# Kernel optimization log

Measured on AMD Instinct MI355X. Metric: run time of the kernel, lower is better.

The kernel has to match this reference:

```python
import jax, jax.numpy as jnp
import numpy as np
import math

B, N, D, H, L, F, K = 4, 256, 768, 32, 12, 3072, 128
HD = D // H
ATOM_TYPES = 64
EDGE_TYPES = ATOM_TYPES * ATOM_TYPES
BLOCKS = 1
SQRT_2PI = math.sqrt(2.0 * math.pi)


def _ln(x, g, b):
    m = jnp.mean(x, -1, keepdims=True)
    v = jnp.mean((x - m) ** 2, -1, keepdims=True)
    return (x - m) * jax.lax.rsqrt(v + 1e-5) * g + b


def _gelu(x):
    return jax.nn.gelu(x, approximate=False)


def setup_inputs():
    key = jax.random.key(0)
    ks = iter(jax.random.split(key, 64))
    def nrm(shape, s=0.02):
        return jax.random.normal(next(ks), shape, jnp.float32) * s
    inp = dict(
        atoms=jax.random.randint(next(ks), (B, N), 0, ATOM_TYPES),
        tags=jax.random.randint(next(ks), (B, N), 0, 3),
        pos=jax.random.normal(next(ks), (B, N, 3), jnp.float32) * 3.0,
        real_mask=jnp.ones((B, N), dtype=bool),
        atom_emb=nrm((ATOM_TYPES, D)),
        tag_emb=nrm((3, D)),
        gbf_means=jax.random.uniform(next(ks), (K,), jnp.float32, 0.0, 3.0),
        gbf_stds=jax.random.uniform(next(ks), (K,), jnp.float32, 0.0, 3.0),
        gbf_mul=jnp.ones((EDGE_TYPES, 1), jnp.float32),
        gbf_bias=jnp.zeros((EDGE_TYPES, 1), jnp.float32),
        bp_w1=nrm((K, K)), bp_b1=jnp.zeros((K,), jnp.float32),
        bp_w2=nrm((H, K)), bp_b2=jnp.zeros((H,), jnp.float32),
        ep_w=nrm((D, K)), ep_b=jnp.zeros((D,), jnp.float32),
        ln1_g=jnp.ones((L, D), jnp.float32), ln1_b=jnp.zeros((L, D), jnp.float32),
        wqkv=nrm((L, 3 * D, D)), bqkv=jnp.zeros((L, 3 * D), jnp.float32),
        wo=nrm((L, D, D)), bo=jnp.zeros((L, D), jnp.float32),
        ln2_g=jnp.ones((L, D), jnp.float32), ln2_b=jnp.zeros((L, D), jnp.float32),
        w1=nrm((L, F, D)), b1=jnp.zeros((L, F), jnp.float32),
        w2=nrm((L, D, F)), b2=jnp.zeros((L, D), jnp.float32),
        fln_g=jnp.ones((D,), jnp.float32), fln_b=jnp.zeros((D,), jnp.float32),
        en_w1=nrm((D, D)), en_b1=jnp.zeros((D,), jnp.float32),
        en_w2=nrm((1, D)), en_b2=jnp.zeros((1,), jnp.float32),
        eagg=nrm((3, 1), 0.01),
        nq_w=nrm((D, D)), nq_b=jnp.zeros((D,), jnp.float32),
        nk_w=nrm((D, D)), nk_b=jnp.zeros((D,), jnp.float32),
        nv_w=nrm((D, D)), nv_b=jnp.zeros((D,), jnp.float32),
        f1_w=nrm((1, D)), f1_b=jnp.zeros((1,), jnp.float32),
        f2_w=nrm((1, D)), f2_b=jnp.zeros((1,), jnp.float32),
        f3_w=nrm((1, D)), f3_b=jnp.zeros((1,), jnp.float32),
    )
    return inp


def _forward(atoms, tags, real_mask, pos, atom_emb, tag_emb, gbf_means, gbf_stds, gbf_mul, gbf_bias,
             bp_w1, bp_b1, bp_w2, bp_b2, ep_w, ep_b,
             ln1_g, ln1_b, wqkv, bqkv, wo, bo, ln2_g, ln2_b, w1, b1, w2, b2,
             fln_g, fln_b, en_w1, en_b1, en_w2, en_b2, eagg,
             nq_w, nq_b, nk_w, nk_b, nv_w, nv_b, f1_w, f1_b, f2_w, f2_b, f3_w, f3_b):
    pad = atoms == 0                                              # [B,N]
    # delta[b,i,j] = pos[b,j] - pos[b,i]  (matches pos.unsqueeze(1) - pos.unsqueeze(2))
    delta = pos[:, None, :, :] - pos[:, :, None, :]               # [B,N,N,3]
    sq = jnp.sum(delta * delta, axis=-1)
    dist = jnp.sqrt(jnp.maximum(sq, 1e-24))                       # safe norm, zero grad on diagonal
    delta = delta / (dist[..., None] + 1e-5)
    edge_type = atoms[:, :, None] * ATOM_TYPES + atoms[:, None, :]  # [B,N,N]
    # Gaussian basis layer
    mul = gbf_mul[edge_type]                                      # [B,N,N,1]
    add = gbf_bias[edge_type]                                     # [B,N,N,1]
    x = mul * dist[..., None] + add                               # [B,N,N,1] -> broadcast to K
    std = jnp.abs(gbf_stds) + 1e-5                                # [K]
    z = (x - gbf_means) / std
    gbf = jnp.exp(-0.5 * z * z) / (SQRT_2PI * std)                # [B,N,N,K]
    edge_feat = jnp.where(pad[:, None, :, None], 0.0, gbf)
    node = tag_emb[tags] + atom_emb[atoms] + (edge_feat.sum(-2) @ ep_w.T + ep_b)  # [B,N,D]
    bias = _gelu(gbf @ bp_w1.T + bp_b1) @ bp_w2.T + bp_b2         # [B,N,N,H]
    bias = jnp.transpose(bias, (0, 3, 1, 2))                      # [B,H,N,N]
    bias = jnp.where(pad[:, None, None, :], -jnp.inf, bias)
    scale = HD ** -0.5
    h = node
    for _ in range(BLOCKS):
        for l in range(L):
            r = h
            y = _ln(h, ln1_g[l], ln1_b[l])
            qkv = y @ wqkv[l].T + bqkv[l]
            q, k, v = jnp.split(qkv, 3, axis=-1)
            q = q.reshape(B, N, H, HD).transpose(0, 2, 1, 3) * scale
            k = k.reshape(B, N, H, HD).transpose(0, 2, 1, 3)
            v = v.reshape(B, N, H, HD).transpose(0, 2, 1, 3)
            a = jnp.einsum('bhid,bhjd->bhij', q, k) + bias
            a = jax.nn.softmax(a, axis=-1)
            o = jnp.einsum('bhij,bhjd->bhid', a, v).transpose(0, 2, 1, 3).reshape(B, N, D)
            h = r + (o @ wo[l].T + bo[l])
            r = h
            y = _ln(h, ln2_g[l], ln2_b[l])
            y = _gelu(y @ w1[l].T + b1[l]) @ w2[l].T + b2[l]
            h = r + y
    out = _ln(h, fln_g, fln_b)                                    # [B,N,D]
    # energy head (eval: no dropout)
    eng = _gelu(out @ en_w1.T + en_b1) @ en_w2.T + en_b2          # [B,N,1]
    eng = (eng * eagg[tags])[..., 0]                              # [B,N]
    omask = (tags > 0) & real_mask
    eng_output = (eng * omask).sum(-1)                            # [B]
    # node task head
    q = (out @ nq_w.T + nq_b).reshape(B, N, H, HD).transpose(0, 2, 1, 3) * scale
    k = (out @ nk_w.T + nk_b).reshape(B, N, H, HD).transpose(0, 2, 1, 3)
    v = (out @ nv_w.T + nv_b).reshape(B, N, H, HD).transpose(0, 2, 1, 3)
    a = jnp.einsum('bhid,bhjd->bhij', q, k) + bias
    a = jax.nn.softmax(a, axis=-1)                                # [B,H,N,N]
    # rot_attn_probs @ v, fused: [b,h,i,j]*[b,i,j,c]*[b,h,j,d] -> [b,i,c,h,d]
    xf = jnp.einsum('bhij,bijc,bhjd->bichd', a, delta, v).reshape(B, N, 3, D)
    f1 = xf[:, :, 0] @ f1_w.T + f1_b
    f2 = xf[:, :, 1] @ f2_w.T + f2_b
    f3 = xf[:, :, 2] @ f3_w.T + f3_b
    node_output = jnp.concatenate([f1, f2, f3], axis=-1)          # [B,N,3]
    return eng_output, node_output, omask[..., None]


def reference(atoms, tags, pos, real_mask, atom_emb, tag_emb, gbf_means, gbf_stds, gbf_mul, gbf_bias,
              bp_w1, bp_b1, bp_w2, bp_b2, ep_w, ep_b,
              ln1_g, ln1_b, wqkv, bqkv, wo, bo, ln2_g, ln2_b, w1, b1, w2, b2,
              fln_g, fln_b, en_w1, en_b1, en_w2, en_b2, eagg,
              nq_w, nq_b, nk_w, nk_b, nv_w, nv_b, f1_w, f1_b, f2_w, f2_b, f3_w, f3_b):
    return _forward(atoms, tags, real_mask, pos, atom_emb, tag_emb, gbf_means, gbf_stds, gbf_mul, gbf_bias,
                    bp_w1, bp_b1, bp_w2, bp_b2, ep_w, ep_b,
                    ln1_g, ln1_b, wqkv, bqkv, wo, bo, ln2_g, ln2_b, w1, b1, w2, b2,
                    fln_g, fln_b, en_w1, en_b1, en_w2, en_b2, eagg,
                    nq_w, nq_b, nk_w, nk_b, nv_w, nv_b, f1_w, f1_b, f2_w, f2_b, f3_w, f3_b)
```

## Files before the change

### kernel.cpp

```cpp
#include <hip/hip_runtime.h>
#include <math.h>

constexpr int B_ = 4, N_ = 256, D_ = 768, H_ = 32, HD_ = 24, L_ = 12, F_ = 3072, K_ = 128;
constexpr float SCALE_ = 0.20412414523193150f;
constexpr float ISQRT2_ = 0.70710678118654752f;

typedef short bf16x8 __attribute__((ext_vector_type(8)));
typedef float f32x4 __attribute__((ext_vector_type(4)));
typedef unsigned short u16x4 __attribute__((ext_vector_type(4)));
typedef unsigned short u16x8 __attribute__((ext_vector_type(8)));
typedef unsigned int u32x4 __attribute__((ext_vector_type(4)));

#define DEV __device__ __forceinline__
#define MFMA16(a, b, c) __builtin_amdgcn_mfma_f32_16x16x32_bf16(a, b, c, 0, 0, 0)

DEV void gload_lds16(const unsigned short* g, unsigned short* l) {
  __builtin_amdgcn_global_load_lds(
      (const __attribute__((address_space(1))) unsigned int*)(g),
      (__attribute__((address_space(3))) unsigned int*)(l), 16, 0, 0);
}

DEV float gelu_f(float x) { return 0.5f * x * (1.0f + erff(x * ISQRT2_)); }

DEV unsigned short f2bf(float f) {
  unsigned u = __float_as_uint(f);
  return (unsigned short)((u + 0x7FFFu + ((u >> 16) & 1u)) >> 16);
}
DEV float bf2f(unsigned short u) { return __uint_as_float(((unsigned)u) << 16); }
DEV unsigned packbf(float a, float b) {
  return (unsigned)f2bf(a) | ((unsigned)f2bf(b) << 16);
}
DEV bf16x8 u4_to_bf8(u32x4 x) { union { u32x4 a; bf16x8 b; } u; u.a = x; return u.b; }

DEV float breduce_sum(float v, float* sred, int tid) {
#pragma unroll
  for (int o = 32; o > 0; o >>= 1) v += __shfl_xor(v, o);
  if ((tid & 63) == 0) sred[tid >> 6] = v;
  __syncthreads();
  v = (sred[0] + sred[1]) + (sred[2] + sred[3]);
  __syncthreads();
  return v;
}

__global__ __launch_bounds__(256) void cast_one_kernel(
    const float* __restrict__ s, unsigned short* __restrict__ d, int n4) {
  const int i = blockIdx.x * 256 + threadIdx.x;
  if (i >= n4) return;
  const float4 v = ((const float4*)s)[i];
  u16x4 o = {f2bf(v.x), f2bf(v.y), f2bf(v.z), f2bf(v.w)};
  ((u16x4*)d)[i] = o;
}

__global__ __launch_bounds__(256) void castlayer_kernel(
    const float* __restrict__ wqkv, const float* __restrict__ wo,
    const float* __restrict__ w1, const float* __restrict__ w2,
    unsigned short* __restrict__ arena) {
  const int i = blockIdx.x * 256 + threadIdx.x;
  const float* s; int j;
  if (i < 442368) { s = wqkv; j = i; }
  else if (i < 589824) { s = wo; j = i - 442368; }
  else if (i < 1179648) { s = w1; j = i - 589824; }
  else { s = w2; j = i - 1179648; }
  const float4 v = ((const float4*)s)[j];
  u16x4 o = {f2bf(v.x), f2bf(v.y), f2bf(v.z), f2bf(v.w)};
  ((u16x4*)arena)[i] = o;
}

__global__ __launch_bounds__(256) void castheads_kernel(
    const float* __restrict__ a, const float* __restrict__ b,
    const float* __restrict__ c, const float* __restrict__ d,
    unsigned short* __restrict__ arena) {
  const int i = blockIdx.x * 256 + threadIdx.x;
  const int r = i / 147456;
  const int j = i - r * 147456;
  const float* s = (r == 0) ? a : (r == 1) ? b : (r == 2) ? c : d;
  const float4 v = ((const float4*)s)[j];
  u16x4 o = {f2bf(v.x), f2bf(v.y), f2bf(v.z), f2bf(v.w)};
  ((u16x4*)arena)[i] = o;
}

__global__ __launch_bounds__(256) void edge_pre_kernel(
    const int* __restrict__ atoms, const float* __restrict__ pos,
    const float* __restrict__ gbf_mul, const float* __restrict__ gbf_bias,
    const float* __restrict__ gbf_means, const float* __restrict__ gbf_stds,
    float* __restrict__ deltaw, float* __restrict__ xvalw, float* __restrict__ nsumw)
{
  const int tid = threadIdx.x;
  const int bi = blockIdx.x;
  const int b = bi >> 8;
  __shared__ float spos[3];
  __shared__ float sxv[256];
  __shared__ int   spad[256];
  __shared__ float red[256];
  if (tid < 3) spos[tid] = pos[(size_t)bi * 3 + tid];
  __syncthreads();
  {
    const int j = tid;
    const float px = pos[(size_t)(b * N_ + j) * 3 + 0];
    const float py = pos[(size_t)(b * N_ + j) * 3 + 1];
    const float pz = pos[(size_t)(b * N_ + j) * 3 + 2];
    const float dx = px - spos[0], dy = py - spos[1], dz = pz - spos[2];
    const float sq = dx * dx + dy * dy + dz * dz;
    const float dist = sqrtf(fmaxf(sq, 1e-24f));
    const float inv = 1.f / (dist + 1e-5f);
    const size_t e = (size_t)bi * N_ + j;
    deltaw[e * 3 + 0] = dx * inv;
    deltaw[e * 3 + 1] = dy * inv;
    deltaw[e * 3 + 2] = dz * inv;
    const int et = atoms[bi] * 64 + atoms[b * N_ + j];
    const float xv = gbf_mul[et] * dist + gbf_bias[et];
    xvalw[e] = xv;
    sxv[j] = xv;
    spad[j] = (atoms[b * N_ + j] == 0);
  }
  __syncthreads();
  const int k = tid & 127;
  const float mean = gbf_means[k];
  const float st = fabsf(gbf_stds[k]) + 1e-5f;
  const float istd = 1.f / st;
  const float coef = 0.39894228040143268f * istd;
  float acc = 0.f;
  const int jbase = tid >> 7;
  for (int t = 0; t < 128; ++t) {
    const int j = jbase + (t << 1);
    if (!spad[j]) {
      const float z = (sxv[j] - mean) * istd;
      acc += expf(-0.5f * z * z) * coef;
    }
  }
  red[tid] = acc;
  __syncthreads();
  if (tid < 128) nsumw[(size_t)bi * K_ + tid] = red[tid] + red[tid + 128];
}

__global__ __launch_bounds__(256) void bias_mfma_kernel(
    const float* __restrict__ xvalw, const int* __restrict__ atoms,
    const float* __restrict__ gbf_means, const float* __restrict__ gbf_stds,
    const unsigned short* __restrict__ w1b, const float* __restrict__ b1,
    const unsigned short* __restrict__ w2b, const float* __restrict__ b2,
    unsigned short* __restrict__ biasb)
{
  __shared__ __align__(16) unsigned short sw1[128 * 128];
  __shared__ __align__(16) unsigned short sw2[32 * 128];
  __shared__ float smean[128], sistd[128], scoef[128], sb1[128], sb2[32];
  const int tid = threadIdx.x;
  const int l = tid & 63;
  const int w = tid >> 6;
  const size_t e0 = (size_t)blockIdx.x * 64;
  const int bB = (int)(e0 >> 16);
  const int iI = (int)((e0 >> 8) & 255);
  const int j0 = (int)(e0 & 255);
  const int lr = l & 15;
  const int lg = l >> 4;

  {
    const int rin = l >> 4;
    const int slot = l & 15;
#pragma unroll
    for (int q = 0; q < 8; ++q) {
      const int rbase = w * 32 + q * 4;
      const int row = rbase + rin;
      const int gs = slot ^ (row & 15);
      gload_lds16(w1b + row * 128 + gs * 8, &sw1[rbase * 128]);
    }
#pragma unroll
    for (int q = 0; q < 2; ++q) {
      const int rbase = w * 8 + q * 4;
      const int row = rbase + rin;
      const int gs = slot ^ (row & 15);
      gload_lds16(w2b + row * 128 + gs * 8, &sw2[rbase * 128]);
    }
  }
  if (tid < 128) {
    const float st = fabsf(gbf_stds[tid]) + 1e-5f;
    const float is = 1.f / st;
    smean[tid] = gbf_means[tid];
    sistd[tid] = is;
    scoef[tid] = 0.39894228040143268f * is;
    sb1[tid] = b1[tid];
  } else if (tid < 160) {
    sb2[tid - 128] = b2[tid - 128];
  }
  const int el = w * 16 + lr;
  const float xv = xvalw[e0 + el];
  const bool padq = (atoms[bB * N_ + j0 + el] == 0);
  __syncthreads();

  bf16x8 bG[4];
#pragma unroll
  for (int ks = 0; ks < 4; ++ks) {
    u16x8 t;
#pragma unroll
    for (int j = 0; j < 8; ++j) {
      const int k = ks * 32 + lg * 8 + j;
      const float z = (xv - smean[k]) * sistd[k];
      t[j] = f2bf(__expf(-0.5f * z * z) * scoef[k]);
    }
    union { u16x8 a; bf16x8 b; } u; u.a = t;
    bG[ks] = u.b;
  }

  f32x4 accM[8];
#pragma unroll
  for (int f = 0; f < 8; ++f) accM[f] = (f32x4)0.f;
#pragma unroll
  for (int ks = 0; ks < 4; ++ks) {
#pragma unroll
    for (int f = 0; f < 8; ++f) {
      const int row = f * 16 + lr;
      const int sl = (ks * 4 + lg) ^ (row & 15);
      const bf16x8 aW = *(const bf16x8*)&sw1[row * 128 + (sl << 3)];
      accM[f] = MFMA16(aW, bG[ks], accM[f]);
    }
  }

  unsigned pm[8][2];
#pragma unroll
  for (int f = 0; f < 8; ++f) {
    float g[4];
#pragma unroll
    for (int r = 0; r < 4; ++r)
      g[r] = gelu_f(accM[f][r] + sb1[f * 16 + lg * 4 + r]);
    pm[f][0] = packbf(g[0], g[1]);
    pm[f][1] = packbf(g[2], g[3]);
  }

  f32x4 accH[2];
  accH[0] = (f32x4)0.f; accH[1] = (f32x4)0.f;
#pragma unroll
  for (int ks = 0; ks < 4; ++ks) {
    const int s0 = ((((lg << 1)) & 3) << 4) + lr;
    const int s1 = ((((lg << 1) + 1) & 3) << 4) + lr;
    const int sel = lg >> 1;
    const unsigned a0 = __shfl(pm[2 * ks][0], s0), b0 = __shfl(pm[2 * ks + 1][0], s0);
    const unsigned a1 = __shfl(pm[2 * ks][1], s0), b1v = __shfl(pm[2 * ks + 1][1], s0);
    const unsigned a2 = __shfl(pm[2 * ks][0], s1), b2v = __shfl(pm[2 * ks + 1][0], s1);
    const unsigned a3 = __shfl(pm[2 * ks][1], s1), b3v = __shfl(pm[2 * ks + 1][1], s1);
    u32x4 bw;
    bw.x = sel ? b0 : a0;
    bw.y = sel ? b1v : a1;
    bw.z = sel ? b2v : a2;
    bw.w = sel ? b3v : a3;
    const bf16x8 bMid = u4_to_bf8(bw);
#pragma unroll
    for (int hf = 0; hf < 2; ++hf) {
      const int row = hf * 16 + lr;
      const int sl = (ks * 4 + lg) ^ (row & 15);
      const bf16x8 aW2 = *(const bf16x8*)&sw2[row * 128 + (sl << 3)];
      accH[hf] = MFMA16(aW2, bMid, accH[hf]);
    }
  }

  const size_t obase = (((size_t)bB * H_) * N_ + iI) * N_ + j0 + el;
#pragma unroll
  for (int hf = 0; hf < 2; ++hf) {
#pragma unroll
    for (int r = 0; r < 4; ++r) {
      const int h = hf * 16 + lg * 4 + r;
      const unsigned short v = padq ? (unsigned short)0xFF80
                                    : f2bf(accH[hf][r] + sb2[h]);
      biasb[obase + (size_t)h * N_ * N_] = v;
    }
  }
}

__global__ __launch_bounds__(256) void node_init_kernel(
    const int* __restrict__ atoms, const int* __restrict__ tags,
    const float* __restrict__ atom_emb, const float* __restrict__ tag_emb,
    const float* __restrict__ nsumw, const float* __restrict__ ep_w,
    const float* __restrict__ ep_b, float* __restrict__ hbuf)
{
  const int bi = blockIdx.x;
  const int tid = threadIdx.x;
  __shared__ float ns[K_];
  if (tid < K_) ns[tid] = nsumw[(size_t)bi * K_ + tid];
  __syncthreads();
  const int at = atoms[bi], tg = tags[bi];
  for (int d = tid; d < D_; d += 256) {
    float acc = tag_emb[tg * D_ + d] + atom_emb[at * D_ + d] + ep_b[d];
    const float* w = ep_w + (size_t)d * K_;
#pragma unroll 8
    for (int kk = 0; kk < K_; ++kk) acc = fmaf(ns[kk], w[kk], acc);
    hbuf[(size_t)bi * D_ + d] = acc;
  }
}

__global__ __launch_bounds__(256) void ln_kernel(
    const float* __restrict__ x, const float* __restrict__ gg,
    const float* __restrict__ bb, unsigned short* __restrict__ y)
{
  const int bi = blockIdx.x;
  const int tid = threadIdx.x;
  __shared__ float sred[4];
  const float* row = x + (size_t)bi * D_;
  const float v0 = row[tid], v1 = row[tid + 256], v2 = row[tid + 512];
  float s = breduce_sum(v0 + v1 + v2, sred, tid);
  const float mean = s * (1.f / 768.f);
  const float d0 = v0 - mean, d1 = v1 - mean, d2 = v2 - mean;
  float q = breduce_sum(d0 * d0 + d1 * d1 + d2 * d2, sred, tid);
  const float inv = rsqrtf(q * (1.f / 768.f) + 1e-5f);
  unsigned short* out = y + (size_t)bi * D_;
  out[tid]       = f2bf(d0 * inv * gg[tid]       + bb[tid]);
  out[tid + 256] = f2bf(d1 * inv * gg[tid + 256] + bb[tid + 256]);
  out[tid + 512] = f2bf(d2 * inv * gg[tid + 512] + bb[tid + 512]);
}

template <int S>
__global__ __launch_bounds__(256) void reduce_ln_kernel(
    const float* __restrict__ P, const float* __restrict__ bias,
    float* __restrict__ hbuf, const float* __restrict__ gg,
    const float* __restrict__ bb, unsigned short* __restrict__ y)
{
  const int row = blockIdx.x;
  const int tid = threadIdx.x;
  __shared__ float sred[4];
  float h[3];
#pragma unroll
  for (int t = 0; t < 3; ++t) {
    const int c = tid + (t << 8);
    float s = bias[c];
#pragma unroll
    for (int z = 0; z < S; ++z)
      s += P[((size_t)z * (B_ * N_) + row) * 768 + c];
    const float hv = hbuf[(size_t)row * 768 + c] + s;
    hbuf[(size_t)row * 768 + c] = hv;
    h[t] = hv;
  }
  float sm = breduce_sum(h[0] + h[1] + h[2], sred, tid);
  const float mean = sm * (1.f / 768.f);
  const float d0 = h[0] - mean, d1 = h[1] - mean, d2 = h[2] - mean;
  float q = breduce_sum(d0 * d0 + d1 * d1 + d2 * d2, sred, tid);
  const float inv = rsqrtf(q * (1.f / 768.f) + 1e-5f);
  unsigned short* out = y + (size_t)row * 768;
  out[tid]       = f2bf(d0 * inv * gg[tid]       + bb[tid]);
  out[tid + 256] = f2bf(d1 * inv * gg[tid + 256] + bb[tid + 256]);
  out[tid + 512] = f2bf(d2 * inv * gg[tid + 512] + bb[tid + 512]);
}

template <int EPI, int OB>
__global__ __launch_bounds__(256) void gemm_mfma(
    const unsigned short* __restrict__ A, const unsigned short* __restrict__ W,
    const float* __restrict__ bias, const float* __restrict__ bias2,
    const float* __restrict__ bias3, const float* __restrict__ bias4,
    float* __restrict__ C, unsigned short* __restrict__ Cb,
    int M, int N, int K, int lda, int ldw)
{
  if (EPI == 4) {
    const int z = blockIdx.z;
    A += (size_t)z * K;
    W += (size_t)z * K;
    C += (size_t)z * M * N;
  }
  __shared__ __align__(16) unsigned short sA[2][64 * 64];
  __shared__ __align__(16) unsigned short sB[2][64 * 64];
  const int tid = threadIdx.x;
  const int l = tid & 63;
  const int w = tid >> 6;
  const int m0 = blockIdx.y * 64;
  const int n0 = blockIdx.x * 64;
  const int wm = w >> 1, wn = w & 1;
  const int lr = l & 15;
  const int lg = l >> 4;
  const int r0 = (w << 4) + (l >> 3);
  const int s0 = (l & 7) ^ (r0 & 7);

  f32x4 acc[2][2];
#pragma unroll
  for (int mi = 0; mi < 2; ++mi)
#pragma unroll
    for (int ni = 0; ni < 2; ++ni) acc[mi][ni] = (f32x4)0.f;

  auto stage = [&](int buf, int t) {
    const size_t kb = (size_t)t << 6;
    unsigned short* lA = &sA[buf][(w << 4) << 6];
    unsigned short* lB = &sB[buf][(w << 4) << 6];
    gload_lds16(A + (size_t)(m0 + r0) * lda + kb + (s0 << 3), lA);
    gload_lds16(A + (size_t)(m0 + r0 + 8) * lda + kb + (s0 << 3), lA + 8 * 64);
    gload_lds16(W + (size_t)(n0 + r0) * ldw + kb + (s0 << 3), lB);
    gload_lds16(W + (size_t)(n0 + r0 + 8) * ldw + kb + (s0 << 3), lB + 8 * 64);
  };

  stage(0, 0);
  const int nt = K >> 6;
  for (int t = 0; t < nt; ++t) {
    __syncthreads();
    if (t + 1 < nt) stage((t + 1) & 1, t + 1);
    const unsigned short* bA = sA[t & 1];
    const unsigned short* bBs = sB[t & 1];
    bf16x8 af[2][2], bfr[2][2];
#pragma unroll
    for (int mi = 0; mi < 2; ++mi) {
      const int row = (wm << 5) + (mi << 4) + lr;
#pragma unroll
      for (int kk = 0; kk < 2; ++kk) {
        const int sl = ((kk << 2) + lg) ^ (row & 7);
        af[mi][kk] = *(const bf16x8*)&bA[(row << 6) + (sl << 3)];
      }
    }
#pragma unroll
    for (int ni = 0; ni < 2; ++ni) {
      const int row = (wn << 5) + (ni << 4) + lr;
#pragma unroll
      for (int kk = 0; kk < 2; ++kk) {
        const int sl = ((kk << 2) + lg) ^ (row & 7);
        bfr[ni][kk] = *(const bf16x8*)&bBs[(row << 6) + (sl << 3)];
      }
    }
#pragma unroll
    for (int kk = 0; kk < 2; ++kk)
#pragma unroll
      for (int mi = 0; mi < 2; ++mi)
#pragma unroll
        for (int ni = 0; ni < 2; ++ni)
          acc[mi][ni] = MFMA16(af[mi][kk], bfr[ni][kk], acc[mi][ni]);
  }

#pragma unroll
  for (int mi = 0; mi < 2; ++mi)
#pragma unroll
    for (int ni = 0; ni < 2; ++ni) {
      const int n = n0 + (wn << 5) + (ni << 4) + lr;
      float bv = 0.f;
      int seg = 0;
      if (EPI == 3) {
        seg = n / 768;
        const float* bp = (seg == 0) ? bias : (seg == 1) ? bias2
                         : (seg == 2) ? bias3 : bias4;
        bv = bp[n - seg * 768];
      } else if (EPI != 4) {
        bv = bias[n];
      }
#pragma unroll
      for (int r = 0; r < 4; ++r) {
        const int m = m0 + (wm << 5) + (mi << 4) + lg * 4 + r;
        float v = acc[mi][ni][r] + bv;
        if (EPI == 1) v = gelu_f(v);
        if (EPI == 3 && seg == 3) v = gelu_f(v);
        if (OB) Cb[(size_t)m * N + n] = f2bf(v);
        else C[(size_t)m * N + n] = v;
      }
    }
}

template <bool PROBS>
__global__ __launch_bounds__(256) void attn_mfma_kernel(
    const unsigned short* __restrict__ Q, const unsigned short* __restrict__ Kp,
    const unsigned short* __restrict__ Vp, const int stride,
    const unsigned short* __restrict__ biasb, unsigned short* __restrict__ obuf,
    unsigned short* __restrict__ aprob)
{
  __shared__ __align__(16) unsigned short sK[256 * 40];
  __shared__ __align__(16) unsigned short sVt[32 * 264];
  __shared__ __align__(16) unsigned short sP[64 * 264];
  const int tid = threadIdx.x;
  const int l = tid & 63, w = tid >> 6;
  const int bh = blockIdx.x, b = bh >> 5, hh = bh & 31;
  const int i0 = blockIdx.y * 64;
  const int lr = l & 15, lg = l >> 4;

#pragma unroll
  for (int it = 0; it < 3; ++it) {
    const int c = tid + (it << 8);
    const int row = c / 3, part = c - row * 3;
    *(u16x8*)&sK[row * 40 + part * 8] =
        *(const u16x8*)&Kp[(size_t)(b * N_ + row) * stride + hh * HD_ + part * 8];
  }
  {
    u16x8 z = {0, 0, 0, 0, 0, 0, 0, 0};
    *(u16x8*)&sK[tid * 40 + 24] = z;
  }
  if (!PROBS) {
    const int j = tid;
    const unsigned short* vr = &Vp[(size_t)(b * N_ + j) * stride + hh * HD_];
    const u16x8 v0 = *(const u16x8*)vr;
    const u16x8 v1 = *(const u16x8*)(vr + 8);
    const u16x8 v2 = *(const u16x8*)(vr + 16);
#pragma unroll
    for (int d = 0; d < 8; ++d) {
      sVt[d * 264 + j] = v0[d];
      sVt[(8 + d) * 264 + j] = v1[d];
      sVt[(16 + d) * 264 + j] = v2[d];
    }
  }
  bf16x8 aQ;
  if (lg < 3) {
    const u16x8 q = *(const u16x8*)&Q[(size_t)(b * N_ + i0 + (w << 4) + lr) * stride + hh * HD_ + lg * 8];
    union { u16x8 a; bf16x8 b; } u; u.a = q;
    aQ = u.b;
  } else {
    bf16x8 t = {0, 0, 0, 0, 0, 0, 0, 0};
    aQ = t;
  }
  __syncthreads();

  f32x4 acc[16];
#pragma unroll
  for (int ni = 0; ni < 16; ++ni) {
    const bf16x8 bK = *(const bf16x8*)&sK[(ni * 16 + lr) * 40 + lg * 8];
    acc[ni] = MFMA16(aQ, bK, (f32x4)0.f);
  }

#pragma unroll
  for (int r = 0; r < 4; ++r) {
    const int iloc = (w << 4) + lg * 4 + r;
    const unsigned short* bp =
        &biasb[(((size_t)(b * H_ + hh)) * N_ + i0 + iloc) * N_ + lr];
    float mx = -INFINITY;
#pragma unroll
    for (int ni = 0; ni < 16; ++ni) {
      const float s = acc[ni][r] * SCALE_ + bf2f(bp[ni * 16]);
      acc[ni][r] = s;
      mx = fmaxf(mx, s);
    }
    mx = fmaxf(mx, __shfl_xor(mx, 1));
    mx = fmaxf(mx, __shfl_xor(mx, 2));
    mx = fmaxf(mx, __shfl_xor(mx, 4));
    mx = fmaxf(mx, __shfl_xor(mx, 8));
    float sum = 0.f;
#pragma unroll
    for (int ni = 0; ni < 16; ++ni) {
      const float e = expf(acc[ni][r] - mx);
      acc[ni][r] = e;
      sum += e;
    }
    sum += __shfl_xor(sum, 1);
    sum += __shfl_xor(sum, 2);
    sum += __shfl_xor(sum, 4);
    sum += __shfl_xor(sum, 8);
    const float inv = 1.f / sum;
#pragma unroll
    for (int ni = 0; ni < 16; ++ni)
      sP[iloc * 264 + ni * 16 + lr] = f2bf(acc[ni][r] * inv);
  }
  __syncthreads();

  if (PROBS) {
#pragma unroll
    for (int it = 0; it < 8; ++it) {
      const int idx = tid + it * 256;
      const int row = idx >> 5, c = idx & 31;
      *(u16x8*)&aprob[(((size_t)(b * H_ + hh)) * N_ + i0 + row) * N_ + c * 8] =
          *(const u16x8*)&sP[row * 264 + c * 8];
    }
  } else {
    f32x4 accO[2];
    accO[0] = (f32x4)0.f; accO[1] = (f32x4)0.f;
#pragma unroll
    for (int ks = 0; ks < 8; ++ks) {
      const bf16x8 aP = *(const bf16x8*)&sP[((w << 4) + lr) * 264 + ks * 32 + lg * 8];
      const bf16x8 bV0 = *(const bf16x8*)&sVt[lr * 264 + ks * 32 + lg * 8];
      const bf16x8 bV1 = *(const bf16x8*)&sVt[(16 + lr) * 264 + ks * 32 + lg * 8];
      accO[0] = MFMA16(aP, bV0, accO[0]);
      accO[1] = MFMA16(aP, bV1, accO[1]);
    }
#pragma unroll
    for (int ni = 0; ni < 2; ++ni) {
      const int n = ni * 16 + lr;
      if (n < HD_) {
#pragma unroll
        for (int r = 0; r < 4; ++r) {
          const int i = i0 + (w << 4) + lg * 4 + r;
          obuf[(size_t)(b * N_ + i) * D_ + hh * HD_ + n] = f2bf(accO[ni][r]);
        }
      }
    }
  }
}

__global__ __launch_bounds__(256) void engnode_kernel(
    const unsigned short* __restrict__ t1, const int stride,
    const float* __restrict__ en_w2, const float* __restrict__ en_b2,
    const float* __restrict__ eagg, const int* __restrict__ tags,
    float* __restrict__ engpn)
{
  const int bi = blockIdx.x;
  const int tid = threadIdx.x;
  __shared__ float sred[4];
  const unsigned short* row = t1 + (size_t)bi * stride;
  float acc = bf2f(row[tid]) * en_w2[tid] + bf2f(row[tid + 256]) * en_w2[tid + 256] +
              bf2f(row[tid + 512]) * en_w2[tid + 512];
  acc = breduce_sum(acc, sred, tid);
  if (tid == 0) {
    const int tg = tags[bi];
    engpn[bi] = (tg > 0) ? (acc + en_b2[0]) * eagg[tg] : 0.f;
  }
}

__global__ __launch_bounds__(256) void engsum_omask_kernel(
    const float* __restrict__ engpn, const int* __restrict__ tags,
    float* __restrict__ out)
{
  const int bid = blockIdx.x;
  const int tid = threadIdx.x;
  if (bid < 4) {
    __shared__ float sred[4];
    float v = breduce_sum(engpn[bid * N_ + tid], sred, tid);
    if (tid == 0) out[bid] = v;
  } else {
    const int idx = (bid - 4) * 256 + tid;
    out[4 + B_ * N_ * 3 + idx] = (tags[idx] > 0) ? 1.f : 0.f;
  }
}

__global__ __launch_bounds__(256) void wv_kernel(
    const unsigned short* __restrict__ vn, const int stride,
    const float* __restrict__ f1w, const float* __restrict__ f2w,
    const float* __restrict__ f3w, float* __restrict__ wv)
{
  const int idx = blockIdx.x * 256 + threadIdx.x;
  const int j = idx & 255;
  const int hh = (idx >> 8) & 31;
  const int b = (idx >> 13) & 3;
  const int c = idx >> 15;
  const float* fw = (c == 0) ? f1w : ((c == 1) ? f2w : f3w);
  const unsigned short* vrow = vn + (size_t)(b * N_ + j) * stride + hh * HD_;
  const u16x8 v0 = *(const u16x8*)vrow;
  const u16x8 v1 = *(const u16x8*)(vrow + 8);
  const u16x8 v2 = *(const u16x8*)(vrow + 16);
  float acc = 0.f;
#pragma unroll
  for (int d = 0; d < 8; ++d) {
    acc = fmaf(bf2f(v0[d]), fw[hh * HD_ + d], acc);
    acc = fmaf(bf2f(v1[d]), fw[hh * HD_ + 8 + d], acc);
    acc = fmaf(bf2f(v2[d]), fw[hh * HD_ + 16 + d], acc);
  }
  wv[idx] = acc;
}

__global__ __launch_bounds__(256) void nodeout_kernel(
    const unsigned short* __restrict__ aprob, const float* __restrict__ wv,
    const float* __restrict__ deltaw, const float* __restrict__ f1b,
    const float* __restrict__ f2b, const float* __restrict__ f3b,
    float* __restrict__ out)
{
  const int bi = blockIdx.x;
  const int c = blockIdx.y;
  const int tid = threadIdx.x;
  const int b = bi >> 8;
  const int i = bi & 255;
  __shared__ float sred[4];
  const unsigned short* ap = aprob + (((size_t)b * H_) * N_ + i) * N_ + tid;
  const float* wvp = wv + ((size_t)(c * B_ + b) * H_) * N_ + tid;
  float s = 0.f;
  for (int hh = 0; hh < H_; ++hh)
    s = fmaf(bf2f(ap[(size_t)hh * N_ * N_]), wvp[(size_t)hh * N_], s);
  s *= deltaw[((size_t)bi * N_ + tid) * 3 + c];
  s = breduce_sum(s, sred, tid);
  if (tid == 0) {
    const float fb = (c == 0) ? f1b[0] : ((c == 1) ? f2b[0] : f3b[0]);
    out[4 + bi * 3 + c] = s + fb;
  }
}

extern "C" void kernel_launch(void* const* d_in, const int* in_sizes, int n_in,
                              void* d_out, int out_size, void* d_ws, size_t ws_size,
                              hipStream_t stream) {
  (void)in_sizes; (void)n_in; (void)out_size; (void)ws_size;
  const int*   atoms     = (const int*)  d_in[0];
  const int*   tags      = (const int*)  d_in[1];
  const float* pos       = (const float*)d_in[2];
  const float* atom_emb  = (const float*)d_in[4];
  const float* tag_emb   = (const float*)d_in[5];
  const float* gbf_means = (const float*)d_in[6];
  const float* gbf_stds  = (const float*)d_in[7];
  const float* gbf_mul   = (const float*)d_in[8];
  const float* gbf_bias  = (const float*)d_in[9];
  const float* bp_w1     = (const float*)d_in[10];
  const float* bp_b1     = (const float*)d_in[11];
  const float* bp_w2     = (const float*)d_in[12];
  const float* bp_b2     = (const float*)d_in[13];
  const float* ep_w      = (const float*)d_in[14];
  const float* ep_b      = (const float*)d_in[15];
  const float* ln1_g     = (const float*)d_in[16];
  const float* ln1_b     = (const float*)d_in[17];
  const float* wqkv      = (const float*)d_in[18];
  const float* bqkv      = (const float*)d_in[19];
  const float* wo        = (const float*)d_in[20];
  const float* bo        = (const float*)d_in[21];
  const float* ln2_g     = (const float*)d_in[22];
  const float* ln2_b     = (const float*)d_in[23];
  const float* w1        = (const float*)d_in[24];
  const float* b1        = (const float*)d_in[25];
  const float* w2        = (const float*)d_in[26];
  const float* b2        = (const float*)d_in[27];
  const float* fln_g     = (const float*)d_in[28];
  const float* fln_b     = (const float*)d_in[29];
  const float* en_w1     = (const float*)d_in[30];
  const float* en_b1     = (const float*)d_in[31];
  const float* en_w2     = (const float*)d_in[32];
  const float* en_b2     = (const float*)d_in[33];
  const float* eagg      = (const float*)d_in[34];
  const float* nq_w      = (const float*)d_in[35];
  const float* nq_b      = (const float*)d_in[36];
  const float* nk_w      = (const float*)d_in[37];
  const float* nk_b      = (const float*)d_in[38];
  const float* nv_w      = (const float*)d_in[39];
  const float* nv_b      = (const float*)d_in[40];
  const float* f1_w      = (const float*)d_in[41];
  const float* f1_b      = (const float*)d_in[42];
  const float* f2_w      = (const float*)d_in[43];
  const float* f2_b      = (const float*)d_in[44];
  const float* f3_w      = (const float*)d_in[45];
  const float* f3_b      = (const float*)d_in[46];

  char* wsB = (char*)d_ws;
  size_t off = 0;
  auto alloc = [&](size_t bytes) {
    void* p = wsB + off;
    off = (off + bytes + 255) & ~(size_t)255;
    return p;
  };
  unsigned short* biasb   = (unsigned short*)alloc((size_t)B_ * H_ * N_ * N_ * 2);
  unsigned short* aprobb  = (unsigned short*)alloc((size_t)B_ * H_ * N_ * N_ * 2);
  float*          deltaw  = (float*)alloc((size_t)B_ * N_ * N_ * 3 * 4);
  float*          xvalw   = (float*)alloc((size_t)B_ * N_ * N_ * 4);
  float*          nsumw   = (float*)alloc((size_t)B_ * N_ * K_ * 4);
  float*          hbuf    = (float*)alloc((size_t)B_ * N_ * D_ * 4);
  unsigned short* qkvb    = (unsigned short*)alloc((size_t)B_ * N_ * 3 * D_ * 2);
  unsigned short* qn4b    = (unsigned short*)alloc((size_t)B_ * N_ * 3072 * 2);
  unsigned short* ybf     = (unsigned short*)alloc((size_t)B_ * N_ * D_ * 2);
  unsigned short* obf     = (unsigned short*)alloc((size_t)B_ * N_ * D_ * 2);
  unsigned short* midbf   = (unsigned short*)alloc((size_t)B_ * N_ * F_ * 2);
  unsigned short* outbf   = (unsigned short*)alloc((size_t)B_ * N_ * D_ * 2);
  unsigned short* arena   = (unsigned short*)alloc((size_t)7077888 * 2);
  unsigned short* headsb  = (unsigned short*)alloc((size_t)2359296 * 2);
  unsigned short* bw1b    = (unsigned short*)alloc((size_t)K_ * K_ * 2);
  unsigned short* bw2b    = (unsigned short*)alloc((size_t)H_ * K_ * 2);
  float*          wopart  = (float*)alloc((size_t)2 * B_ * N_ * D_ * 4);
  float*          ffpart  = (float*)alloc((size_t)4 * B_ * N_ * D_ * 4);
  float*          wvb     = (float*)alloc((size_t)3 * B_ * H_ * N_ * 4);
  float*          engpn   = (float*)alloc((size_t)B_ * N_ * 4);

  const int BN = B_ * N_;
  float* outp = (float*)d_out;
  const size_t OQKV = 0, OWO = 1769472, OW1 = 2359296, OW2 = 4718592;

  edge_pre_kernel<<<BN, 256, 0, stream>>>(atoms, pos, gbf_mul, gbf_bias,
                                          gbf_means, gbf_stds, deltaw, xvalw, nsumw);
  cast_one_kernel<<<16, 256, 0, stream>>>(bp_w1, bw1b, 4096);
  cast_one_kernel<<<4, 256, 0, stream>>>(bp_w2, bw2b, 1024);
  bias_mfma_kernel<<<B_ * N_ * N_ / 64, 256, 0, stream>>>(
      xvalw, atoms, gbf_means, gbf_stds, bw1b, bp_b1, bw2b, bp_b2, biasb);
  node_init_kernel<<<BN, 256, 0, stream>>>(atoms, tags, atom_emb, tag_emb,
                                           nsumw, ep_w, ep_b, hbuf);
  ln_kernel<<<BN, 256, 0, stream>>>(hbuf, ln1_g, ln1_b, ybf);

  for (int l = 0; l < L_; ++l) {
    castlayer_kernel<<<6912, 256, 0, stream>>>(
        wqkv + (size_t)l * 3 * D_ * D_, wo + (size_t)l * D_ * D_,
        w1 + (size_t)l * F_ * D_, w2 + (size_t)l * D_ * F_, arena);
    gemm_mfma<0, 1><<<dim3(36, 16), 256, 0, stream>>>(
        ybf, arena + OQKV, bqkv + (size_t)l * 3 * D_, nullptr, nullptr, nullptr,
        nullptr, qkvb, BN, 3 * D_, D_, D_, D_);
    attn_mfma_kernel<false><<<dim3(B_ * H_, 4), 256, 0, stream>>>(
        qkvb, qkvb + D_, qkvb + 2 * D_, 3 * D_, biasb, obf, nullptr);
    gemm_mfma<4, 0><<<dim3(12, 16, 2), 256, 0, stream>>>(
        obf, arena + OWO, nullptr, nullptr, nullptr, nullptr,
        wopart, nullptr, BN, D_, 384, D_, D_);
    reduce_ln_kernel<2><<<BN, 256, 0, stream>>>(
        wopart, bo + (size_t)l * D_, hbuf, ln2_g + (size_t)l * D_,
        ln2_b + (size_t)l * D_, ybf);
    gemm_mfma<1, 1><<<dim3(48, 16), 256, 0, stream>>>(
        ybf, arena + OW1, b1 + (size_t)l * F_, nullptr, nullptr, nullptr,
        nullptr, midbf, BN, F_, D_, D_, D_);
    gemm_mfma<4, 0><<<dim3(12, 16, 4), 256, 0, stream>>>(
        midbf, arena + OW2, nullptr, nullptr, nullptr, nullptr,
        ffpart, nullptr, BN, D_, 768, F_, F_);
    const bool last = (l == L_ - 1);
    reduce_ln_kernel<4><<<BN, 256, 0, stream>>>(
        ffpart, b2 + (size_t)l * D_, hbuf,
        last ? fln_g : ln1_g + (size_t)(l + 1) * D_,
        last ? fln_b : ln1_b + (size_t)(l + 1) * D_,
        last ? outbf : ybf);
  }

  castheads_kernel<<<2304, 256, 0, stream>>>(nq_w, nk_w, nv_w, en_w1, headsb);

  gemm_mfma<3, 1><<<dim3(48, 16), 256, 0, stream>>>(
      outbf, headsb, nq_b, nk_b, nv_b, en_b1,
      nullptr, qn4b, BN, 3072, D_, D_, D_);

  attn_mfma_kernel<true><<<dim3(B_ * H_, 4), 256, 0, stream>>>(
      qn4b, qn4b + 768, qn4b + 1536, 3072, biasb, nullptr, aprobb);
  wv_kernel<<<3 * B_ * H_ * N_ / 256, 256, 0, stream>>>(
      qn4b + 1536, 3072, f1_w, f2_w, f3_w, wvb);
  nodeout_kernel<<<dim3(BN, 3), 256, 0, stream>>>(aprobb, wvb, deltaw,
                                                  f1_b, f2_b, f3_b, outp);

  engnode_kernel<<<BN, 256, 0, stream>>>(qn4b + 2304, 3072, en_w2, en_b2,
                                         eagg, tags, engpn);
  engsum_omask_kernel<<<8, 256, 0, stream>>>(engpn, tags, outp);
}
```

Before: 1.078 ms.

## Fuse fp32-to-bf16 weight conversion into GEMM B-tile staging

Removes the per-layer castlayer and castheads kernels and has the GEMM load fp32 weights directly into registers, converting them to bf16 and writing them into swizzled LDS after the MFMAs. This saves the separate cast pass (an fp32 read plus a bf16 write and read back) and its launches. In exchange, every M-tile block now reads fp32 weights, so weight global traffic per GEMM doubles and is repeated across 16 row blocks. The register-path loads are also no longer asynchronous direct-to-LDS loads.

```diff
diff --git a/kernel.cpp b/kernel.cpp
--- a/kernel.cpp
+++ b/kernel.cpp
@@ -31,6 +31,11 @@
   return (unsigned)f2bf(a) | ((unsigned)f2bf(b) << 16);
 }
 DEV bf16x8 u4_to_bf8(u32x4 x) { union { u32x4 a; bf16x8 b; } u; u.a = x; return u.b; }
+DEV bf16x8 cvt8(const float4 a, const float4 b) {
+  u16x8 t = {f2bf(a.x), f2bf(a.y), f2bf(a.z), f2bf(a.w),
+             f2bf(b.x), f2bf(b.y), f2bf(b.z), f2bf(b.w)};
+  union { u16x8 u; bf16x8 s; } uu; uu.u = t; return uu.s;
+}
 
 DEV float breduce_sum(float v, float* sred, int tid) {
 #pragma unroll
@@ -49,34 +54,6 @@
   const float4 v = ((const float4*)s)[i];
   u16x4 o = {f2bf(v.x), f2bf(v.y), f2bf(v.z), f2bf(v.w)};
   ((u16x4*)d)[i] = o;
-}
-
-__global__ __launch_bounds__(256) void castlayer_kernel(
-    const float* __restrict__ wqkv, const float* __restrict__ wo,
-    const float* __restrict__ w1, const float* __restrict__ w2,
-    unsigned short* __restrict__ arena) {
-  const int i = blockIdx.x * 256 + threadIdx.x;
-  const float* s; int j;
-  if (i < 442368) { s = wqkv; j = i; }
-  else if (i < 589824) { s = wo; j = i - 442368; }
-  else if (i < 1179648) { s = w1; j = i - 589824; }
-  else { s = w2; j = i - 1179648; }
-  const float4 v = ((const float4*)s)[j];
-  u16x4 o = {f2bf(v.x), f2bf(v.y), f2bf(v.z), f2bf(v.w)};
-  ((u16x4*)arena)[i] = o;
-}
-
-__global__ __launch_bounds__(256) void castheads_kernel(
-    const float* __restrict__ a, const float* __restrict__ b,
-    const float* __restrict__ c, const float* __restrict__ d,
-    unsigned short* __restrict__ arena) {
-  const int i = blockIdx.x * 256 + threadIdx.x;
-  const int r = i / 147456;
-  const int j = i - r * 147456;
-  const float* s = (r == 0) ? a : (r == 1) ? b : (r == 2) ? c : d;
-  const float4 v = ((const float4*)s)[j];
-  u16x4 o = {f2bf(v.x), f2bf(v.y), f2bf(v.z), f2bf(v.w)};
-  ((u16x4*)arena)[i] = o;
 }
 
 __global__ __launch_bounds__(256) void edge_pre_kernel(
@@ -339,16 +316,29 @@
 
 template <int EPI, int OB>
 __global__ __launch_bounds__(256) void gemm_mfma(
-    const unsigned short* __restrict__ A, const unsigned short* __restrict__ W,
+    const unsigned short* __restrict__ A,
+    const float* __restrict__ Wa, const float* __restrict__ Wb,
+    const float* __restrict__ Wc, const float* __restrict__ Wd,
     const float* __restrict__ bias, const float* __restrict__ bias2,
     const float* __restrict__ bias3, const float* __restrict__ bias4,
     float* __restrict__ C, unsigned short* __restrict__ Cb,
     int M, int N, int K, int lda, int ldw)
 {
+  const int n0 = blockIdx.x * 64;
+  const float* Wp;
+  int nb;
+  if (EPI == 3) {
+    const int seg = n0 / 768;
+    Wp = (seg == 0) ? Wa : (seg == 1) ? Wb : (seg == 2) ? Wc : Wd;
+    nb = n0 - seg * 768;
+  } else {
+    Wp = Wa;
+    nb = n0;
+  }
   if (EPI == 4) {
     const int z = blockIdx.z;
     A += (size_t)z * K;
-    W += (size_t)z * K;
+    Wp += (size_t)z * K;
     C += (size_t)z * M * N;
   }
   __shared__ __align__(16) unsigned short sA[2][64 * 64];
@@ -357,12 +347,16 @@
   const int l = tid & 63;
   const int w = tid >> 6;
   const int m0 = blockIdx.y * 64;
-  const int n0 = blockIdx.x * 64;
   const int wm = w >> 1, wn = w & 1;
   const int lr = l & 15;
   const int lg = l >> 4;
   const int r0 = (w << 4) + (l >> 3);
   const int s0 = (l & 7) ^ (r0 & 7);
+  const int brow0 = tid >> 3;
+  const int bslot = tid & 7;
+  const int bgs0 = bslot ^ (brow0 & 7);
+  const int brow1 = 32 + brow0;
+  const int bgs1 = bslot ^ (brow1 & 7);
 
   f32x4 acc[2][2];
 #pragma unroll
@@ -370,21 +364,32 @@
 #pragma unroll
     for (int ni = 0; ni < 2; ++ni) acc[mi][ni] = (f32x4)0.f;
 
-  auto stage = [&](int buf, int t) {
+  float4 w00, w01, w10, w11;
+  auto issueW = [&](int t) {
+    const float* p0 = Wp + (size_t)(nb + brow0) * ldw + ((size_t)t << 6) + (bgs0 << 3);
+    const float* p1 = Wp + (size_t)(nb + brow1) * ldw + ((size_t)t << 6) + (bgs1 << 3);
+    w00 = *(const float4*)p0; w01 = *(const float4*)(p0 + 4);
+    w10 = *(const float4*)p1; w11 = *(const float4*)(p1 + 4);
+  };
+  auto writeW = [&](int buf) {
+    *(bf16x8*)&sB[buf][tid * 8] = cvt8(w00, w01);
+    *(bf16x8*)&sB[buf][2048 + tid * 8] = cvt8(w10, w11);
+  };
+  auto gloadA = [&](int buf, int t) {
     const size_t kb = (size_t)t << 6;
     unsigned short* lA = &sA[buf][(w << 4) << 6];
-    unsigned short* lB = &sB[buf][(w << 4) << 6];
     gload_lds16(A + (size_t)(m0 + r0) * lda + kb + (s0 << 3), lA);
     gload_lds16(A + (size_t)(m0 + r0 + 8) * lda + kb + (s0 << 3), lA + 8 * 64);
-    gload_lds16(W + (size_t)(n0 + r0) * ldw + kb + (s0 << 3), lB);
-    gload_lds16(W + (size_t)(n0 + r0 + 8) * ldw + kb + (s0 << 3), lB + 8 * 64);
   };
 
-  stage(0, 0);
   const int nt = K >> 6;
+  issueW(0);
+  gloadA(0, 0);
+  writeW(0);
   for (int t = 0; t < nt; ++t) {
     __syncthreads();
-    if (t + 1 < nt) stage((t + 1) & 1, t + 1);
+    const bool pf = (t + 1 < nt);
+    if (pf) { issueW(t + 1); gloadA((t + 1) & 1, t + 1); }
     const unsigned short* bA = sA[t & 1];
     const unsigned short* bBs = sB[t & 1];
     bf16x8 af[2][2], bfr[2][2];
@@ -413,6 +418,7 @@
 #pragma unroll
         for (int ni = 0; ni < 2; ++ni)
           acc[mi][ni] = MFMA16(af[mi][kk], bfr[ni][kk], acc[mi][ni]);
+    if (pf) writeW((t + 1) & 1);
   }
 
 #pragma unroll
@@ -722,8 +728,6 @@
   unsigned short* obf     = (unsigned short*)alloc((size_t)B_ * N_ * D_ * 2);
   unsigned short* midbf   = (unsigned short*)alloc((size_t)B_ * N_ * F_ * 2);
   unsigned short* outbf   = (unsigned short*)alloc((size_t)B_ * N_ * D_ * 2);
-  unsigned short* arena   = (unsigned short*)alloc((size_t)7077888 * 2);
-  unsigned short* headsb  = (unsigned short*)alloc((size_t)2359296 * 2);
   unsigned short* bw1b    = (unsigned short*)alloc((size_t)K_ * K_ * 2);
   unsigned short* bw2b    = (unsigned short*)alloc((size_t)H_ * K_ * 2);
   float*          wopart  = (float*)alloc((size_t)2 * B_ * N_ * D_ * 4);
@@ -733,7 +737,6 @@
 
   const int BN = B_ * N_;
   float* outp = (float*)d_out;
-  const size_t OQKV = 0, OWO = 1769472, OW1 = 2359296, OW2 = 4718592;
 
   edge_pre_kernel<<<BN, 256, 0, stream>>>(atoms, pos, gbf_mul, gbf_bias,
                                           gbf_means, gbf_stds, deltaw, xvalw, nsumw);
@@ -746,25 +749,26 @@
   ln_kernel<<<BN, 256, 0, stream>>>(hbuf, ln1_g, ln1_b, ybf);
 
   for (int l = 0; l < L_; ++l) {
-    castlayer_kernel<<<6912, 256, 0, stream>>>(
-        wqkv + (size_t)l * 3 * D_ * D_, wo + (size_t)l * D_ * D_,
-        w1 + (size_t)l * F_ * D_, w2 + (size_t)l * D_ * F_, arena);
     gemm_mfma<0, 1><<<dim3(36, 16), 256, 0, stream>>>(
-        ybf, arena + OQKV, bqkv + (size_t)l * 3 * D_, nullptr, nullptr, nullptr,
+        ybf, wqkv + (size_t)l * 3 * D_ * D_, nullptr, nullptr, nullptr,
+        bqkv + (size_t)l * 3 * D_, nullptr, nullptr, nullptr,
         nullptr, qkvb, BN, 3 * D_, D_, D_, D_);
     attn_mfma_kernel<false><<<dim3(B_ * H_, 4), 256, 0, stream>>>(
         qkvb, qkvb + D_, qkvb + 2 * D_, 3 * D_, biasb, obf, nullptr);
     gemm_mfma<4, 0><<<dim3(12, 16, 2), 256, 0, stream>>>(
-        obf, arena + OWO, nullptr, nullptr, nullptr, nullptr,
+        obf, wo + (size_t)l * D_ * D_, nullptr, nullptr, nullptr,
+        nullptr, nullptr, nullptr, nullptr,
         wopart, nullptr, BN, D_, 384, D_, D_);
     reduce_ln_kernel<2><<<BN, 256, 0, stream>>>(
         wopart, bo + (size_t)l * D_, hbuf, ln2_g + (size_t)l * D_,
         ln2_b + (size_t)l * D_, ybf);
     gemm_mfma<1, 1><<<dim3(48, 16), 256, 0, stream>>>(
-        ybf, arena + OW1, b1 + (size_t)l * F_, nullptr, nullptr, nullptr,
+        ybf, w1 + (size_t)l * F_ * D_, nullptr, nullptr, nullptr,
+        b1 + (size_t)l * F_, nullptr, nullptr, nullptr,
         nullptr, midbf, BN, F_, D_, D_, D_);
     gemm_mfma<4, 0><<<dim3(12, 16, 4), 256, 0, stream>>>(
-        midbf, arena + OW2, nullptr, nullptr, nullptr, nullptr,
+        midbf, w2 + (size_t)l * D_ * F_, nullptr, nullptr, nullptr,
+        nullptr, nullptr, nullptr, nullptr,
         ffpart, nullptr, BN, D_, 768, F_, F_);
     const bool last = (l == L_ - 1);
     reduce_ln_kernel<4><<<BN, 256, 0, stream>>>(
@@ -774,10 +778,9 @@
         last ? outbf : ybf);
   }
 
-  castheads_kernel<<<2304, 256, 0, stream>>>(nq_w, nk_w, nv_w, en_w1, headsb);
-
   gemm_mfma<3, 1><<<dim3(48, 16), 256, 0, stream>>>(
-      outbf, headsb, nq_b, nk_b, nv_b, en_b1,
+      outbf, nq_w, nk_w, nv_w, en_w1,
+      nq_b, nk_b, nv_b, en_b1,
       nullptr, qn4b, BN, 3072, D_, D_, D_);
 
   attn_mfma_kernel<true><<<dim3(B_ * H_, 4), 256, 0, stream>>>(
```

Measured after the change: 1.168 ms. +8.3%, slower.
